# Kernel tuning notes

Hardware: AMD Instinct MI355X
Metric: run time of the kernel (lower is better)

Reference implementation:

```python
import jax, jax.numpy as jnp
import numpy as np

N = 100000
E = 640000
ND = 128   # node_dim
ED = 128   # edge_dim
HD = 256   # hidden_dim
EPS = 1e-5


def _mlp_ln(x, W1, b1, W2, b2, W3, b3, g, beta):
    h = jax.nn.relu(x @ W1 + b1)
    h = jax.nn.relu(h @ W2 + b2)
    o = h @ W3 + b3
    mu = jnp.mean(o, axis=-1, keepdims=True)
    var = jnp.mean(jnp.square(o - mu), axis=-1, keepdims=True)
    return (o - mu) * jax.lax.rsqrt(var + EPS) * g + beta


def setup_inputs() -> dict:
    key = jax.random.key(0)
    ks = jax.random.split(key, 20)
    s = 0.02
    inp = {
        "node_emb": jax.random.normal(ks[0], (N, ND), jnp.float32),
        "edge_emb": jax.random.normal(ks[1], (E, ED), jnp.float32),
        "src": jax.random.randint(ks[2], (E,), 0, N),
        "dst": jax.random.randint(ks[3], (E,), 0, N),
        "num_nodes": N,
        # edge MLP: in = 2*ND + ED
        "eW1": jax.random.normal(ks[4], (2 * ND + ED, HD), jnp.float32) * s,
        "eb1": jnp.zeros((HD,), jnp.float32),
        "eW2": jax.random.normal(ks[5], (HD, HD), jnp.float32) * s,
        "eb2": jnp.zeros((HD,), jnp.float32),
        "eW3": jax.random.normal(ks[6], (HD, ED), jnp.float32) * s,
        "eb3": jnp.zeros((ED,), jnp.float32),
        "eg": jnp.ones((ED,), jnp.float32),
        "ebeta": jnp.zeros((ED,), jnp.float32),
        # node MLP: in = ND + ED
        "nW1": jax.random.normal(ks[7], (ND + ED, HD), jnp.float32) * s,
        "nb1": jnp.zeros((HD,), jnp.float32),
        "nW2": jax.random.normal(ks[8], (HD, HD), jnp.float32) * s,
        "nb2": jnp.zeros((HD,), jnp.float32),
        "nW3": jax.random.normal(ks[9], (HD, ND), jnp.float32) * s,
        "nb3": jnp.zeros((ND,), jnp.float32),
        "ng": jnp.ones((ND,), jnp.float32),
        "nbeta": jnp.zeros((ND,), jnp.float32),
    }
    return inp


def reference(node_emb, edge_emb, src, dst, num_nodes,
              eW1, eb1, eW2, eb2, eW3, eb3, eg, ebeta,
              nW1, nb1, nW2, nb2, nW3, nb3, ng, nbeta):
    # Edge update: e' = MLP(concat(h_i, h_j, e)) + e
    edge_input = jnp.concatenate([node_emb[src], node_emb[dst], edge_emb], axis=-1)
    edge_emb_new = _mlp_ln(edge_input, eW1, eb1, eW2, eb2, eW3, eb3, eg, ebeta) + edge_emb
    # Mean aggregation over incoming edges per dst node
    agg = jax.ops.segment_sum(edge_emb_new, dst, num_segments=num_nodes)
    count = jax.ops.segment_sum(jnp.ones((dst.shape[0], 1), node_emb.dtype), dst, num_segments=num_nodes)
    agg = agg / jnp.maximum(count, 1.0)
    # Node update: h' = MLP(concat(h, agg)) + h
    node_input = jnp.concatenate([node_emb, agg], axis=-1)
    node_emb_new = _mlp_ln(node_input, nW1, nb1, nW2, nb2, nW3, nb3, ng, nbeta) + node_emb
    return (node_emb_new, edge_emb_new)
```

## Files before the change

kernel.cpp:

```cpp
#include <hip/hip_runtime.h>
#include <hip/hip_bf16.h>

typedef __attribute__((ext_vector_type(8))) short bf16x8;
typedef __attribute__((ext_vector_type(4))) short s16x4;
typedef __attribute__((ext_vector_type(4))) float f32x4;

__device__ __forceinline__ short f2bf(float f) {
  union { __hip_bfloat16 h; short s; } u;
  u.h = __float2bfloat16(f);
  return u.s;
}

__device__ __forceinline__ void gld_lds16(const short* g, short* l) {
  __builtin_amdgcn_global_load_lds((const __attribute__((address_space(1))) unsigned*)g,
                                   (__attribute__((address_space(3))) unsigned*)l,
                                   16, 0, 0);
}

#define BARX(N) asm volatile("s_waitcnt vmcnt(" #N ") lgkmcnt(0)\ns_barrier" ::: "memory")
#define BARLG() asm volatile("s_waitcnt lgkmcnt(0)\ns_barrier" ::: "memory")

__global__ void cvt_kernel(const float* __restrict__ in, short* __restrict__ out, long n8) {
  long i = (long)blockIdx.x * blockDim.x + threadIdx.x;
  const long stride = (long)gridDim.x * blockDim.x;
  for (; i < n8; i += stride) {
    const float* p = in + i * 8;
    float4 a = *(const float4*)p, b = *(const float4*)(p + 4);
    bf16x8 o;
    o[0] = f2bf(a.x); o[1] = f2bf(a.y); o[2] = f2bf(a.z); o[3] = f2bf(a.w);
    o[4] = f2bf(b.x); o[5] = f2bf(b.y); o[6] = f2bf(b.z); o[7] = f2bf(b.w);
    *(bf16x8*)(out + i * 8) = o;
  }
}

template <bool PERM>
__global__ void prep_kernel(const float* __restrict__ W, short* __restrict__ out, int K, int N) {
  int s = blockIdx.x * 256 + threadIdx.x;
  int NF = N >> 4;
  int total = (K >> 5) * NF * 64;
  if (s >= total) return;
  int l = s & 63, kcf = s >> 6;
  int kc = kcf / NF, f = kcf - kc * NF;
  int kg = l >> 4, l16 = l & 15;
  bf16x8 o;
#pragma unroll
  for (int e = 0; e < 8; ++e) {
    int kh = kc * 32 + kg * 8 + e;
    int k = PERM ? ((kh & ~63) | ((kh & 3) << 4) | ((kh >> 2) & 15)) : kh;
    o[e] = f2bf(W[(size_t)k * N + f * 16 + l16]);
  }
  *(bf16x8*)(out + (size_t)s * 8) = o;
}

__global__ void count_kernel(const int* __restrict__ dst, int* __restrict__ cnt, int E) {
  int i = blockIdx.x * 256 + threadIdx.x;
  if (i < E) atomicAdd(&cnt[dst[i]], 1);
}

__global__ void bsum_kernel(const int* __restrict__ cnt, int* __restrict__ bsum, int N) {
  __shared__ int wsum[4];
  int b = blockIdx.x, t = threadIdx.x;
  int base = b * 2048;
  int s = 0;
#pragma unroll
  for (int j = 0; j < 8; ++j) {
    int i = base + j * 256 + t;
    s += (i < N) ? cnt[i] : 0;
  }
#pragma unroll
  for (int m = 1; m < 64; m <<= 1) s += __shfl_xor(s, m);
  if ((t & 63) == 0) wsum[t >> 6] = s;
  __syncthreads();
  if (t == 0) bsum[b] = wsum[0] + wsum[1] + wsum[2] + wsum[3];
}

__global__ void bscan_kernel(int* __restrict__ bsum, int nb) {
  int l = threadIdx.x;
  int v = (l < nb) ? bsum[l] : 0;
  int x = v;
#pragma unroll
  for (int d = 1; d < 64; d <<= 1) { int y = __shfl_up(x, d); if (l >= d) x += y; }
  if (l < nb) bsum[l] = x - v;
}

__global__ void offs_kernel(const int* __restrict__ cnt, const int* __restrict__ bsum,
                            int* __restrict__ off, int* __restrict__ cursor, int N) {
  __shared__ int wpre[4];
  int b = blockIdx.x, t = threadIdx.x, w = t >> 6, l = t & 63;
  int base = b * 2048;
  int v[8];
  int s = 0;
#pragma unroll
  for (int j = 0; j < 8; ++j) {
    int i = base + t * 8 + j;
    v[j] = (i < N) ? cnt[i] : 0;
    s += v[j];
  }
  int x = s;
#pragma unroll
  for (int d = 1; d < 64; d <<= 1) { int y = __shfl_up(x, d); if (l >= d) x += y; }
  if (l == 63) wpre[w] = x;
  __syncthreads();
  int wo = 0;
  for (int k = 0; k < w; ++k) wo += wpre[k];
  int excl = bsum[b] + wo + x - s;
#pragma unroll
  for (int j = 0; j < 8; ++j) {
    int i = base + t * 8 + j;
    if (i < N) { off[i] = excl; cursor[i] = excl; }
    excl += v[j];
  }
  if (b == gridDim.x - 1 && t == 255) off[N] = excl;
}

__global__ void scatter_kernel(const int* __restrict__ dst, int* __restrict__ cursor,
                               int* __restrict__ eidx, int E) {
  int e = blockIdx.x * 256 + threadIdx.x;
  if (e < E) {
    int p = atomicAdd(&cursor[dst[e]], 1);
    eidx[p] = e;
  }
}

__global__ void agg_kernel(const float* __restrict__ edge_out, const int* __restrict__ eidx,
                           const int* __restrict__ off, short* __restrict__ aggb, int N) {
  int n = blockIdx.x * 4 + (threadIdx.x >> 6);
  if (n >= N) return;
  int l = threadIdx.x & 63;
  int beg = off[n], end = off[n + 1];
  float ax = 0.f, ay = 0.f;
  int i = beg;
  for (; i + 4 <= end; i += 4) {
    int e0 = eidx[i], e1 = eidx[i + 1], e2 = eidx[i + 2], e3 = eidx[i + 3];
    float2 v0 = *(const float2*)(edge_out + (size_t)e0 * 128 + l * 2);
    float2 v1 = *(const float2*)(edge_out + (size_t)e1 * 128 + l * 2);
    float2 v2 = *(const float2*)(edge_out + (size_t)e2 * 128 + l * 2);
    float2 v3 = *(const float2*)(edge_out + (size_t)e3 * 128 + l * 2);
    ax += v0.x + v1.x + v2.x + v3.x;
    ay += v0.y + v1.y + v2.y + v3.y;
  }
  for (; i < end; ++i) {
    int e = eidx[i];
    float2 v = *(const float2*)(edge_out + (size_t)e * 128 + l * 2);
    ax += v.x; ay += v.y;
  }
  float inv = 1.0f / fmaxf((float)(end - beg), 1.0f);
  unsigned pk = ((unsigned)(unsigned short)f2bf(ay * inv) << 16) |
                (unsigned)(unsigned short)f2bf(ax * inv);
  *(unsigned*)&aggb[(size_t)n * 128 + l * 2] = pk;
}

struct F8 { float4 a, b; };

template <bool IS_EDGE>
__launch_bounds__(512)
__global__ void mlp_kernel(const float* __restrict__ node_emb_f, const float* __restrict__ edge_emb_f,
                           const short* __restrict__ node_bf, const short* __restrict__ agg_bf,
                           const int* __restrict__ src, const int* __restrict__ dst,
                           const short* __restrict__ wAll,
                           const float* __restrict__ b1, const float* __restrict__ b2,
                           const float* __restrict__ b3,
                           const float* __restrict__ gam, const float* __restrict__ bet,
                           float* __restrict__ out_base, int M) {
  extern __shared__ short smem[];
  short* Bs = smem;
  short* Hs = smem + 24576;

  const int tid = threadIdx.x;
  const int m0 = blockIdx.x * 128;
  const int w = tid >> 6, lane = tid & 63, l16 = lane & 15, kg = lane >> 4;
  const int wr = w >> 2, wc = w & 3;

  constexpr int NL1 = IS_EDGE ? 12 : 8;

  const int grow = ((tid >> 6) & 7) * 16 + (tid & 15);
  const int gcq = ((tid >> 4) & 3) * 8;
  const int grc = min(m0 + grow, M - 1);
  int gsr = 0, gdr = 0;
  if (IS_EDGE) { gsr = src[grc]; gdr = dst[grc]; }

  float b1v[4], b2v[4];
#pragma unroll
  for (int ct = 0; ct < 4; ++ct) {
    int col = wc * 64 + ct * 16 + l16;
    b1v[ct] = b1[col];
    b2v[ct] = b2[col];
  }
  float b3v[8], gv[8], bev[8];
#pragma unroll
  for (int f = 0; f < 8; ++f) {
    int col = f * 16 + l16;
    b3v[f] = b3[col]; gv[f] = gam[col]; bev[f] = bet[col];
  }

  f32x4 acc[16];
#pragma unroll
  for (int i = 0; i < 16; ++i) { f32x4 z = {0.f, 0.f, 0.f, 0.f}; acc[i] = z; }

  auto stageW = [&](int v) {
    const short* g = wAll + (size_t)v * 8192;
    short* l = Bs + (size_t)(v % 3) * 8192;
    gld_lds16(g + (size_t)tid * 8, l + (size_t)tid * 8);
    gld_lds16(g + (size_t)(tid + 512) * 8, l + (size_t)(tid + 512) * 8);
  };
  auto stageAb = [&](int v) {
    short* dstp = Hs + (size_t)(v % 3) * 4096 + (size_t)tid * 8;
    int col = v * 32 + gcq;
    const short* q;
    if (IS_EDGE) {
      q = node_bf + (size_t)(col < 128 ? gsr : gdr) * 128 + (col & 127);
    } else {
      q = (col < 128) ? node_bf + (size_t)grc * 128 + col
                      : agg_bf + (size_t)grc * 128 + (col - 128);
    }
    gld_lds16(q, dstp);
  };
  auto loadAf = [&](int v) -> F8 {
    const float* q = edge_emb_f + (size_t)grc * 128 + (v * 32 + gcq - 256);
    F8 r;
    r.a = *(const float4*)q;
    r.b = *(const float4*)(q + 4);
    return r;
  };
  auto storeAf = [&](int v, const F8& p) {
    float t[8];
    *(float4*)t = p.a; *(float4*)(t + 4) = p.b;
    bf16x8 o;
#pragma unroll
    for (int e = 0; e < 8; ++e) o[e] = f2bf(t[e]);
    *(bf16x8*)(Hs + (size_t)(v % 3) * 4096 + (size_t)tid * 8) = o;
  };

  auto compA = [&](int u) {
    const short* Ap = Hs + (size_t)(u % 3) * 4096;
    const short* Bp = Bs + (size_t)(u % 3) * 8192;
    bf16x8 a[4], b[4];
#pragma unroll
    for (int rt = 0; rt < 4; ++rt)
      a[rt] = *(const bf16x8*)&Ap[(size_t)((wr * 4 + rt) * 64 + lane) * 8];
#pragma unroll
    for (int ct = 0; ct < 4; ++ct)
      b[ct] = *(const bf16x8*)&Bp[(size_t)((wc * 4 + ct) * 64 + lane) * 8];
#pragma unroll
    for (int rt = 0; rt < 4; ++rt)
#pragma unroll
      for (int ct = 0; ct < 4; ++ct)
        acc[rt * 4 + ct] = __builtin_amdgcn_mfma_f32_16x16x32_bf16(a[rt], b[ct], acc[rt * 4 + ct], 0, 0, 0);
  };

  auto compH = [&](int kc, const short* Bp) {
    bf16x8 a[4], b[4];
#pragma unroll
    for (int rt = 0; rt < 4; ++rt) {
      int row = wr * 64 + rt * 16 + l16;
      int ch = (kc * 32 + kg * 8) ^ ((row & 7) << 3);
      a[rt] = *(const bf16x8*)&Hs[(size_t)row * 256 + ch];
    }
#pragma unroll
    for (int ct = 0; ct < 4; ++ct)
      b[ct] = *(const bf16x8*)&Bp[(size_t)((wc * 4 + ct) * 64 + lane) * 8];
#pragma unroll
    for (int rt = 0; rt < 4; ++rt)
#pragma unroll
      for (int ct = 0; ct < 4; ++ct)
        acc[rt * 4 + ct] = __builtin_amdgcn_mfma_f32_16x16x32_bf16(a[rt], b[ct], acc[rt * 4 + ct], 0, 0, 0);
  };

  auto writeH = [&](const float* bv) {
#pragma unroll
    for (int rt = 0; rt < 4; ++rt)
#pragma unroll
      for (int q = 0; q < 4; ++q) {
        int row = wr * 64 + rt * 16 + kg * 4 + q;
        s16x4 v;
#pragma unroll
        for (int ct = 0; ct < 4; ++ct)
          v[ct] = f2bf(fmaxf(acc[rt * 4 + ct][q] + bv[ct], 0.f));
        int ch = (wc * 64 + l16 * 4) ^ ((row & 7) << 3);
        *(s16x4*)&Hs[(size_t)row * 256 + ch] = v;
      }
#pragma unroll
    for (int i = 0; i < 16; ++i) { f32x4 z = {0.f, 0.f, 0.f, 0.f}; acc[i] = z; }
  };

  auto compL3 = [&](int kk, const short* Bp) {
    int row = w * 16 + l16;
    int ch = (kk * 32 + kg * 8) ^ ((row & 7) << 3);
    bf16x8 a = *(const bf16x8*)&Hs[(size_t)row * 256 + ch];
    const short* Bsub = Bp + (size_t)(kk & 1) * 4096;
#pragma unroll
    for (int f = 0; f < 8; ++f) {
      bf16x8 b = *(const bf16x8*)&Bsub[(size_t)(f * 64 + lane) * 8];
      acc[f] = __builtin_amdgcn_mfma_f32_16x16x32_bf16(a, b, acc[f], 0, 0, 0);
    }
  };

  stageW(0);
  stageAb(0);
  stageW(1);
  stageAb(1);
  BARX(3);

#pragma unroll 1
  for (int u = 0; u < 6; ++u) {
    stageW(u + 2);
    stageAb(u + 2);
    compA(u);
    BARX(3);
  }

  if (IS_EDGE) {
#pragma unroll 1
    for (int u = 6; u < 10; ++u) {
      F8 p = loadAf(u + 2);
      stageW(u + 2);
      compA(u);
      storeAf(u + 2, p);
      BARX(2);
    }
  }

#pragma unroll 1
  for (int u = NL1 - 2; u < NL1; ++u) {
    stageW(u + 2);
    compA(u);
    BARX(2);
  }
  writeH(b1v);
  BARLG();

#pragma unroll 1
  for (int u = NL1; u < NL1 + 8; ++u) {
    stageW(u + 2);
    compH(u - NL1, Bs + (size_t)(u % 3) * 8192);
    BARX(2);
  }
  writeH(b2v);
  BARLG();

  {
    const int us = NL1 + 8;
#pragma unroll 1
    for (int k = 0; k < 2; ++k) {
      int u = us + k;
      stageW(u + 2);
      const short* Bp = Bs + (size_t)(u % 3) * 8192;
      compL3(2 * k, Bp);
      compL3(2 * k + 1, Bp);
      BARX(2);
    }
    {
      const short* Bp = Bs + (size_t)((us + 2) % 3) * 8192;
      compL3(4, Bp);
      compL3(5, Bp);
      BARX(0);
    }
    {
      const short* Bp = Bs + (size_t)((us + 3) % 3) * 8192;
      compL3(6, Bp);
      compL3(7, Bp);
    }
  }

#pragma unroll
  for (int q = 0; q < 4; ++q) {
    int rg = m0 + w * 16 + kg * 4 + q;
    float o[8], s1 = 0.f, s2 = 0.f;
#pragma unroll
    for (int f = 0; f < 8; ++f) {
      float x = acc[f][q] + b3v[f];
      o[f] = x; s1 += x; s2 += x * x;
    }
#pragma unroll
    for (int m = 1; m <= 8; m <<= 1) { s1 += __shfl_xor(s1, m); s2 += __shfl_xor(s2, m); }
    float mu = s1 * (1.f / 128.f);
    float var = s2 * (1.f / 128.f) - mu * mu;
    float rs = rsqrtf(var + 1e-5f);
    if (rg < M) {
      const float* resid = (IS_EDGE ? edge_emb_f : node_emb_f) + (size_t)rg * 128;
      float* op = out_base + (size_t)rg * 128;
#pragma unroll
      for (int f = 0; f < 8; ++f) {
        int col = f * 16 + l16;
        op[col] = (o[f] - mu) * rs * gv[f] + bev[f] + resid[col];
      }
    }
  }
}

extern "C" void kernel_launch(void* const* d_in, const int* in_sizes, int n_in,
                              void* d_out, int out_size, void* d_ws, size_t ws_size,
                              hipStream_t stream) {
  const float* node_emb = (const float*)d_in[0];
  const float* edge_emb = (const float*)d_in[1];
  const int*   src      = (const int*)d_in[2];
  const int*   dst      = (const int*)d_in[3];
  const float* eW1 = (const float*)d_in[5];
  const float* eb1 = (const float*)d_in[6];
  const float* eW2 = (const float*)d_in[7];
  const float* eb2 = (const float*)d_in[8];
  const float* eW3 = (const float*)d_in[9];
  const float* eb3 = (const float*)d_in[10];
  const float* eg  = (const float*)d_in[11];
  const float* ebt = (const float*)d_in[12];
  const float* nW1 = (const float*)d_in[13];
  const float* nb1 = (const float*)d_in[14];
  const float* nW2 = (const float*)d_in[15];
  const float* nb2 = (const float*)d_in[16];
  const float* nW3 = (const float*)d_in[17];
  const float* nb3 = (const float*)d_in[18];
  const float* ng  = (const float*)d_in[19];
  const float* nbt = (const float*)d_in[20];

  const int Nn = in_sizes[0] / 128;
  const int Ee = in_sizes[2];
  const int nb2048 = (Nn + 2047) / 2048;

  char* ws = (char*)d_ws;
  short* aggb   = (short*)ws;  ws += (size_t)Nn * 128 * 2;
  short* nodebf = (short*)ws;  ws += (size_t)Nn * 128 * 2;
  int* cnt_i  = (int*)ws;      ws += (size_t)Nn * 4;
  int* cursor = (int*)ws;      ws += (size_t)Nn * 4;
  int* offv   = (int*)ws;      ws += (size_t)(Nn + 1) * 4;
  int* eidx   = (int*)ws;      ws += (size_t)Ee * 4;
  int* bsum   = (int*)ws;      ws += 64 * 4;
  ws = (char*)(((uintptr_t)ws + 15) & ~(uintptr_t)15);
  short* eAll = (short*)ws;
  short* nAll = eAll + 196608;

  float* out_node = (float*)d_out;
  float* out_edge = out_node + (size_t)Nn * 128;

  hipMemsetAsync(cnt_i, 0, (size_t)Nn * 4, stream);

  cvt_kernel<<<2048, 256, 0, stream>>>(node_emb, nodebf, (long)Nn * 16);

  prep_kernel<false><<<48, 256, 0, stream>>>(eW1, eAll, 384, 256);
  prep_kernel<true><<<32, 256, 0, stream>>>(eW2, eAll + 98304, 256, 256);
  prep_kernel<true><<<16, 256, 0, stream>>>(eW3, eAll + 163840, 256, 128);
  prep_kernel<false><<<32, 256, 0, stream>>>(nW1, nAll, 256, 256);
  prep_kernel<true><<<32, 256, 0, stream>>>(nW2, nAll + 65536, 256, 256);
  prep_kernel<true><<<16, 256, 0, stream>>>(nW3, nAll + 131072, 256, 128);

  count_kernel<<<(Ee + 255) / 256, 256, 0, stream>>>(dst, cnt_i, Ee);
  bsum_kernel<<<nb2048, 256, 0, stream>>>(cnt_i, bsum, Nn);
  bscan_kernel<<<1, 64, 0, stream>>>(bsum, nb2048);
  offs_kernel<<<nb2048, 256, 0, stream>>>(cnt_i, bsum, offv, cursor, Nn);
  scatter_kernel<<<(Ee + 255) / 256, 256, 0, stream>>>(dst, cursor, eidx, Ee);

  mlp_kernel<true><<<(Ee + 127) / 128, 512, 114688, stream>>>(
      node_emb, edge_emb, nodebf, aggb, src, dst, eAll,
      eb1, eb2, eb3, eg, ebt, out_edge, Ee);

  agg_kernel<<<(Nn + 3) / 4, 256, 0, stream>>>(out_edge, eidx, offv, aggb, Nn);

  mlp_kernel<false><<<(Nn + 127) / 128, 512, 114688, stream>>>(
      node_emb, edge_emb, nodebf, aggb, src, dst, nAll,
      nb1, nb2, nb3, ng, nbt, out_node, Nn);
}
```

Measured before the change: 673.3 us.

## Emit bf16 edge copy for aggregation gather and merge small prep kernels

The edge MLP now also writes a bf16 copy of its output into workspace when space allows, and the aggregation kernel gathers those half-size rows instead of the fp32 output. The separate count kernel is folded into the node conversion kernel, and the six weight-prep launches become one kernel. The aim is to halve the random-gather traffic in aggregation and cut launch overhead. The cost is an extra 2-byte scalar store per element in the edge epilogue (about 164 MB more written) and bf16 rounding of the values that get averaged.

```diff
diff --git a/kernel.cpp b/kernel.cpp
--- a/kernel.cpp
+++ b/kernel.cpp
@@ -20,10 +20,11 @@
 #define BARX(N) asm volatile("s_waitcnt vmcnt(" #N ") lgkmcnt(0)\ns_barrier" ::: "memory")
 #define BARLG() asm volatile("s_waitcnt lgkmcnt(0)\ns_barrier" ::: "memory")
 
-__global__ void cvt_kernel(const float* __restrict__ in, short* __restrict__ out, long n8) {
-  long i = (long)blockIdx.x * blockDim.x + threadIdx.x;
-  const long stride = (long)gridDim.x * blockDim.x;
-  for (; i < n8; i += stride) {
+__global__ void cvt_count_kernel(const float* __restrict__ in, short* __restrict__ out, long n8,
+                                 const int* __restrict__ dst, int* __restrict__ cnt, int E) {
+  const long T = (long)gridDim.x * blockDim.x;
+  const long t0 = (long)blockIdx.x * blockDim.x + threadIdx.x;
+  for (long i = t0; i < n8; i += T) {
     const float* p = in + i * 8;
     float4 a = *(const float4*)p, b = *(const float4*)(p + 4);
     bf16x8 o;
@@ -31,11 +32,22 @@
     o[4] = f2bf(b.x); o[5] = f2bf(b.y); o[6] = f2bf(b.z); o[7] = f2bf(b.w);
     *(bf16x8*)(out + i * 8) = o;
   }
-}
-
-template <bool PERM>
-__global__ void prep_kernel(const float* __restrict__ W, short* __restrict__ out, int K, int N) {
-  int s = blockIdx.x * 256 + threadIdx.x;
+  for (long j = t0; j < E; j += T) atomicAdd(&cnt[dst[j]], 1);
+}
+
+__global__ void prep_all_kernel(const float* __restrict__ eW1, const float* __restrict__ eW2,
+                                const float* __restrict__ eW3, const float* __restrict__ nW1,
+                                const float* __restrict__ nW2, const float* __restrict__ nW3,
+                                short* __restrict__ eAll, short* __restrict__ nAll) {
+  int b = blockIdx.x;
+  const float* W; short* out; int K, N; bool perm;
+  if (b < 48)       { W = eW1; out = eAll;          K = 384; N = 256; perm = false; }
+  else if (b < 80)  { W = eW2; out = eAll + 98304;  K = 256; N = 256; perm = true;  b -= 48; }
+  else if (b < 96)  { W = eW3; out = eAll + 163840; K = 256; N = 128; perm = true;  b -= 80; }
+  else if (b < 128) { W = nW1; out = nAll;          K = 256; N = 256; perm = false; b -= 96; }
+  else if (b < 160) { W = nW2; out = nAll + 65536;  K = 256; N = 256; perm = true;  b -= 128; }
+  else              { W = nW3; out = nAll + 131072; K = 256; N = 128; perm = true;  b -= 160; }
+  int s = b * 256 + threadIdx.x;
   int NF = N >> 4;
   int total = (K >> 5) * NF * 64;
   if (s >= total) return;
@@ -46,15 +58,10 @@
 #pragma unroll
   for (int e = 0; e < 8; ++e) {
     int kh = kc * 32 + kg * 8 + e;
-    int k = PERM ? ((kh & ~63) | ((kh & 3) << 4) | ((kh >> 2) & 15)) : kh;
+    int k = perm ? ((kh & ~63) | ((kh & 3) << 4) | ((kh >> 2) & 15)) : kh;
     o[e] = f2bf(W[(size_t)k * N + f * 16 + l16]);
   }
   *(bf16x8*)(out + (size_t)s * 8) = o;
-}
-
-__global__ void count_kernel(const int* __restrict__ dst, int* __restrict__ cnt, int E) {
-  int i = blockIdx.x * 256 + threadIdx.x;
-  if (i < E) atomicAdd(&cnt[dst[i]], 1);
 }
 
 __global__ void bsum_kernel(const int* __restrict__ cnt, int* __restrict__ bsum, int N) {
@@ -122,8 +129,10 @@
   }
 }
 
-__global__ void agg_kernel(const float* __restrict__ edge_out, const int* __restrict__ eidx,
-                           const int* __restrict__ off, short* __restrict__ aggb, int N) {
+template <bool BF>
+__global__ void agg_kernel(const float* __restrict__ edge_out, const short* __restrict__ edge_bf,
+                           const int* __restrict__ eidx, const int* __restrict__ off,
+                           short* __restrict__ aggb, int N) {
   int n = blockIdx.x * 4 + (threadIdx.x >> 6);
   if (n >= N) return;
   int l = threadIdx.x & 63;
@@ -131,18 +140,29 @@
   float ax = 0.f, ay = 0.f;
   int i = beg;
   for (; i + 4 <= end; i += 4) {
-    int e0 = eidx[i], e1 = eidx[i + 1], e2 = eidx[i + 2], e3 = eidx[i + 3];
-    float2 v0 = *(const float2*)(edge_out + (size_t)e0 * 128 + l * 2);
-    float2 v1 = *(const float2*)(edge_out + (size_t)e1 * 128 + l * 2);
-    float2 v2 = *(const float2*)(edge_out + (size_t)e2 * 128 + l * 2);
-    float2 v3 = *(const float2*)(edge_out + (size_t)e3 * 128 + l * 2);
-    ax += v0.x + v1.x + v2.x + v3.x;
-    ay += v0.y + v1.y + v2.y + v3.y;
+#pragma unroll
+    for (int j = 0; j < 4; ++j) {
+      int e = eidx[i + j];
+      if (BF) {
+        unsigned v = *(const unsigned*)(edge_bf + (size_t)e * 128 + l * 2);
+        ax += __uint_as_float(v << 16);
+        ay += __uint_as_float(v & 0xffff0000u);
+      } else {
+        float2 v = *(const float2*)(edge_out + (size_t)e * 128 + l * 2);
+        ax += v.x; ay += v.y;
+      }
+    }
   }
   for (; i < end; ++i) {
     int e = eidx[i];
-    float2 v = *(const float2*)(edge_out + (size_t)e * 128 + l * 2);
-    ax += v.x; ay += v.y;
+    if (BF) {
+      unsigned v = *(const unsigned*)(edge_bf + (size_t)e * 128 + l * 2);
+      ax += __uint_as_float(v << 16);
+      ay += __uint_as_float(v & 0xffff0000u);
+    } else {
+      float2 v = *(const float2*)(edge_out + (size_t)e * 128 + l * 2);
+      ax += v.x; ay += v.y;
+    }
   }
   float inv = 1.0f / fmaxf((float)(end - beg), 1.0f);
   unsigned pk = ((unsigned)(unsigned short)f2bf(ay * inv) << 16) |
@@ -161,7 +181,7 @@
                            const float* __restrict__ b1, const float* __restrict__ b2,
                            const float* __restrict__ b3,
                            const float* __restrict__ gam, const float* __restrict__ bet,
-                           float* __restrict__ out_base, int M) {
+                           float* __restrict__ out_base, short* __restrict__ out_bf, int M) {
   extern __shared__ short smem[];
   short* Bs = smem;
   short* Hs = smem + 24576;
@@ -382,7 +402,9 @@
 #pragma unroll
       for (int f = 0; f < 8; ++f) {
         int col = f * 16 + l16;
-        op[col] = (o[f] - mu) * rs * gv[f] + bev[f] + resid[col];
+        float y = (o[f] - mu) * rs * gv[f] + bev[f] + resid[col];
+        op[col] = y;
+        if (IS_EDGE && out_bf) out_bf[(size_t)rg * 128 + col] = f2bf(y);
       }
     }
   }
@@ -416,7 +438,8 @@
   const int Ee = in_sizes[2];
   const int nb2048 = (Nn + 2047) / 2048;
 
-  char* ws = (char*)d_ws;
+  char* ws0 = (char*)d_ws;
+  char* ws = ws0;
   short* aggb   = (short*)ws;  ws += (size_t)Nn * 128 * 2;
   short* nodebf = (short*)ws;  ws += (size_t)Nn * 128 * 2;
   int* cnt_i  = (int*)ws;      ws += (size_t)Nn * 4;
@@ -427,22 +450,20 @@
   ws = (char*)(((uintptr_t)ws + 15) & ~(uintptr_t)15);
   short* eAll = (short*)ws;
   short* nAll = eAll + 196608;
+  char* after = (char*)(nAll + 163840);
+  after = (char*)(((uintptr_t)after + 15) & ~(uintptr_t)15);
+  short* edge_bf = nullptr;
+  if ((size_t)(after - ws0) + (size_t)Ee * 128 * 2 <= ws_size)
+    edge_bf = (short*)after;
 
   float* out_node = (float*)d_out;
   float* out_edge = out_node + (size_t)Nn * 128;
 
   hipMemsetAsync(cnt_i, 0, (size_t)Nn * 4, stream);
 
-  cvt_kernel<<<2048, 256, 0, stream>>>(node_emb, nodebf, (long)Nn * 16);
-
-  prep_kernel<false><<<48, 256, 0, stream>>>(eW1, eAll, 384, 256);
-  prep_kernel<true><<<32, 256, 0, stream>>>(eW2, eAll + 98304, 256, 256);
-  prep_kernel<true><<<16, 256, 0, stream>>>(eW3, eAll + 163840, 256, 128);
-  prep_kernel<false><<<32, 256, 0, stream>>>(nW1, nAll, 256, 256);
-  prep_kernel<true><<<32, 256, 0, stream>>>(nW2, nAll + 65536, 256, 256);
-  prep_kernel<true><<<16, 256, 0, stream>>>(nW3, nAll + 131072, 256, 128);
-
-  count_kernel<<<(Ee + 255) / 256, 256, 0, stream>>>(dst, cnt_i, Ee);
+  cvt_count_kernel<<<2048, 256, 0, stream>>>(node_emb, nodebf, (long)Nn * 16, dst, cnt_i, Ee);
+  prep_all_kernel<<<176, 256, 0, stream>>>(eW1, eW2, eW3, nW1, nW2, nW3, eAll, nAll);
+
   bsum_kernel<<<nb2048, 256, 0, stream>>>(cnt_i, bsum, Nn);
   bscan_kernel<<<1, 64, 0, stream>>>(bsum, nb2048);
   offs_kernel<<<nb2048, 256, 0, stream>>>(cnt_i, bsum, offv, cursor, Nn);
@@ -450,11 +471,14 @@
 
   mlp_kernel<true><<<(Ee + 127) / 128, 512, 114688, stream>>>(
       node_emb, edge_emb, nodebf, aggb, src, dst, eAll,
-      eb1, eb2, eb3, eg, ebt, out_edge, Ee);
-
-  agg_kernel<<<(Nn + 3) / 4, 256, 0, stream>>>(out_edge, eidx, offv, aggb, Nn);
+      eb1, eb2, eb3, eg, ebt, out_edge, edge_bf, Ee);
+
+  if (edge_bf)
+    agg_kernel<true><<<(Nn + 3) / 4, 256, 0, stream>>>(out_edge, edge_bf, eidx, offv, aggb, Nn);
+  else
+    agg_kernel<false><<<(Nn + 3) / 4, 256, 0, stream>>>(out_edge, edge_bf, eidx, offv, aggb, Nn);
 
   mlp_kernel<false><<<(Nn + 127) / 128, 512, 114688, stream>>>(
       node_emb, edge_emb, nodebf, aggb, src, dst, nAll,
-      nb1, nb2, nb3, ng, nbt, out_node, Nn);
-}
+      nb1, nb2, nb3, ng, nbt, out_node, nullptr, Nn);
+}
```

Result: slower. 742.7 us (+10.3%).
